# Kernel optimization log

Measured on AMD Instinct MI355X. Metric: run time of the kernel, lower is better.

## Reference

```python
import jax, jax.numpy as jnp
import numpy as np

MAJOR = 100          # major_resolution
SAMPLE = 11          # sample_resolution (11x11 = 121 blur taps)
SCALE = 1.0          # sample_scale
N_SIGMA = 4.0
B, C, H, W = 16, 3, 256, 256


def _gaussian_blur_grid(n):
    # torch.linspace(-1,1,n+2)[1:-1], meshgrid indexing 'ij'
    lin = jnp.linspace(-1.0, 1.0, n + 2)[1:-1]
    xx, yy = jnp.meshgrid(lin, lin, indexing='ij')
    ww = jnp.exp(-0.5 * (xx * xx + yy * yy) * N_SIGMA ** 2)
    ww = ww / jnp.sum(ww)
    return xx.ravel(), yy.ravel(), ww.ravel()


def _grid_sample_bilinear_zeros(x, grid):
    """torch.nn.functional.grid_sample, mode='bilinear', padding_mode='zeros',
    align_corners=False. x: [B,C,H,W], grid: [B,Ho,Wo,2] (last dim = (x,y))."""
    _, _, h, w = x.shape
    # unnormalize (align_corners=False): pixel = ((g+1)*size - 1)/2
    ix = ((grid[..., 0] + 1.0) * w - 1.0) * 0.5
    iy = ((grid[..., 1] + 1.0) * h - 1.0) * 0.5
    ix0 = jnp.floor(ix)
    iy0 = jnp.floor(iy)
    ix1 = ix0 + 1.0
    iy1 = iy0 + 1.0
    wx1 = ix - ix0
    wx0 = 1.0 - wx1
    wy1 = iy - iy0
    wy0 = 1.0 - wy1

    def tap(iy_f, ix_f, wgt):
        valid = ((iy_f >= 0) & (iy_f <= h - 1) & (ix_f >= 0) & (ix_f <= w - 1)).astype(x.dtype)
        iyc = jnp.clip(iy_f.astype(jnp.int32), 0, h - 1)
        ixc = jnp.clip(ix_f.astype(jnp.int32), 0, w - 1)
        # gather per batch element: [C,H,W] indexed by [Ho,Wo] -> [C,Ho,Wo]
        g = jax.vmap(lambda img, a, b: img[:, a, b])(x, iyc, ixc)  # [B,C,Ho,Wo]
        return g * (wgt * valid)[:, None, :, :]

    return (tap(iy0, ix0, wy0 * wx0) + tap(iy0, ix1, wy0 * wx1)
            + tap(iy1, ix0, wy1 * wx0) + tap(iy1, ix1, wy1 * wx1))


def setup_inputs() -> dict:
    key = jax.random.key(0)
    k1, k2 = jax.random.split(key)
    x = jax.random.normal(k1, (B, C, H, W), dtype=jnp.float32)
    theta = jax.random.normal(k2, (B, 2, 3), dtype=jnp.float32)
    return {"x": x, "theta": theta}


def reference(x, theta):
    b, c, _, _ = x.shape
    m = MAJOR
    bx, by, bw = _gaussian_blur_grid(SAMPLE)
    scale = SCALE / (m - 1)
    # affine_grid base coords, align_corners=False pixel centers in [-1,1]
    lin = (jnp.arange(m, dtype=x.dtype) + 0.5) * (2.0 / m) - 1.0
    coords = jnp.stack([
        jnp.broadcast_to(lin[None, :], (m, m)),   # x varies along width
        jnp.broadcast_to(lin[:, None], (m, m)),   # y varies along height
        jnp.ones((m, m), x.dtype),
    ], axis=-1)  # [M,M,3]

    def step(acc, tap):
        dx, dy, wgt = tap
        # _shift_affine_grid: theta[:,:,2] += theta[:,:,0]*dx + theta[:,:,1]*dy
        th = theta.at[:, :, 2].add(theta[:, :, 0] * (dx * scale) + theta[:, :, 1] * (dy * scale))
        grid = jnp.einsum('bij,hwj->bhwi', th, coords)  # [B,M,M,2]
        acc = acc + wgt * _grid_sample_bilinear_zeros(x, grid)
        return acc, None

    out0 = jnp.zeros((b, c, m, m), x.dtype)
    out, _ = jax.lax.scan(step, out0, (bx, by, bw))
    return out
```

## Files before the change

kernel.cpp:

```cpp
#include <hip/hip_runtime.h>
#include <hip/hip_fp16.h>


#define BB 16
#define HWP 65536
#define SMEMN 3072

__device__ const unsigned char KEPT[112] = {
    2,   3,   4,   5,   6,   7,   8,
    12,  13,  14,  15,  16,  17,  18,  19,  20,
    22,  23,  24,  25,  26,  27,  28,  29,  30,  31,  32,
    33,  34,  35,  36,  37,  38,  39,  40,  41,  42,  43,
    44,  45,  46,  47,  48,  49,  50,  51,  52,  53,  54,
    55,  56,  57,  58,  59,  60,  61,  62,  63,  64,  65,
    66,  67,  68,  69,  70,  71,  72,  73,  74,  75,  76,
    77,  78,  79,  80,  81,  82,  83,  84,  85,  86,  87,
    88,  89,  90,  91,  92,  93,  94,  95,  96,  97,  98,
    100, 101, 102, 103, 104, 105, 106, 107, 108,
    112, 113, 114, 115, 116, 117, 118,
    255, 255, 255};

#define INV_SUMW 0.07076221f
#define PXSCALE 1.2929293f

__global__ __launch_bounds__(256) void stn_fused(const float* __restrict__ x,
                                                 const float* __restrict__ theta,
                                                 float* __restrict__ out) {
  __shared__ uint2 smem[SMEMN];

  int bid = blockIdx.x;
  int swz = (bid & 7) * 1250 + (bid >> 3);
  int tid = threadIdx.x;
  int sub = tid & 15;
  int grp = tid >> 4;

  int b = swz / 625;
  int tt = swz - b * 625;
  int ti = tt / 25, tj = tt - ti * 25;
  int i0 = ti * 4, j0 = tj * 4;
  int i = i0 + (grp >> 2), j = j0 + (grp & 3);

  const float* th = theta + b * 6;
  float th00 = th[0], th01 = th[1], th02 = th[2];
  float th10 = th[3], th11 = th[4], th12 = th[5];

  float linj = (j + 0.5f) * 0.02f - 1.0f;
  float lini = (i + 0.5f) * 0.02f - 1.0f;
  float bix = (th00 * linj + th01 * lini + th02) * 128.0f + 127.5f;
  float biy = (th10 * linj + th11 * lini + th12) * 128.0f + 127.5f;

  float lj0 = (j0 + 0.5f) * 0.02f - 1.0f, lj3 = (j0 + 3.5f) * 0.02f - 1.0f;
  float li0 = (i0 + 0.5f) * 0.02f - 1.0f, li3 = (i0 + 3.5f) * 0.02f - 1.0f;
  float cx00 = th00 * lj0 + th01 * li0, cx01 = th00 * lj3 + th01 * li0;
  float cx10 = th00 * lj0 + th01 * li3, cx11 = th00 * lj3 + th01 * li3;
  float cy00 = th10 * lj0 + th11 * li0, cy01 = th10 * lj3 + th11 * li0;
  float cy10 = th10 * lj0 + th11 * li3, cy11 = th10 * lj3 + th11 * li3;
  float bxm = (fminf(fminf(cx00, cx01), fminf(cx10, cx11)) + th02) * 128.0f + 127.5f;
  float bxM = (fmaxf(fmaxf(cx00, cx01), fmaxf(cx10, cx11)) + th02) * 128.0f + 127.5f;
  float bym = (fminf(fminf(cy00, cy01), fminf(cy10, cy11)) + th12) * 128.0f + 127.5f;
  float byM = (fmaxf(fmaxf(cy00, cy01), fmaxf(cy10, cy11)) + th12) * 128.0f + 127.5f;
  float rx = 1.0775f * (fabsf(th00) + fabsf(th01));
  float ry = 1.0775f * (fabsf(th10) + fabsf(th11));
  int X0 = (int)floorf(bxm - rx) - 1;
  int X1 = (int)floorf(bxM + rx) + 2;
  int Y0 = (int)floorf(bym - ry) - 1;
  int Y1 = (int)floorf(byM + ry) + 2;
  int wreg = X1 - X0 + 1, hreg = Y1 - Y0 + 1;
  bool fast = (wreg <= 64) && (hreg <= 96) && (wreg * hreg <= SMEMN);

  float a00 = th00 * PXSCALE, a01 = th01 * PXSCALE;
  float a10 = th10 * PXSCALE, a11 = th11 * PXSCALE;
  float offx[7], offy[7], wk[7];
#pragma unroll
  for (int k = 0; k < 7; ++k) {
    int t = KEPT[sub + 16 * k];
    float dxk = 0.f, dyk = 0.f, wkk = 0.f;
    if (t != 255) {
      int s = t / 11, u = t - s * 11;
      dxk = (float)(s + 1) * 0.16666667f - 1.0f;
      dyk = (float)(u + 1) * 0.16666667f - 1.0f;
      wkk = __expf(-8.0f * (dxk * dxk + dyk * dyk)) * INV_SUMW;
    }
    offx[k] = a00 * dxk + a01 * dyk;
    offy[k] = a10 * dxk + a11 * dyk;
    wk[k] = wkk;
  }

  float acc0 = 0.f, acc1 = 0.f, acc2 = 0.f;
  const float* xb = x + (size_t)b * 3 * HWP;

  if (fast) {
    int c = tid & 63;
    for (int r = tid >> 6; r < hreg; r += 4) {
      if (c < wreg) {
        int py = Y0 + r, px = X0 + c;
        float v0 = 0.f, v1 = 0.f, v2 = 0.f;
        if ((unsigned)py < 256u && (unsigned)px < 256u) {
          int o = py * 256 + px;
          v0 = xb[o];
          v1 = xb[o + HWP];
          v2 = xb[o + 2 * HWP];
        }
        uint2 pkd;
        pkd.x = __builtin_bit_cast(unsigned, __floats2half2_rn(v0, v1));
        pkd.y = __builtin_bit_cast(unsigned, __floats2half2_rn(v2, 0.f));
        smem[r * wreg + c] = pkd;
      }
    }
    __syncthreads();

#pragma unroll
    for (int k = 0; k < 7; ++k) {
      float ixf = bix + offx[k];
      float iyf = biy + offy[k];
      float xf0 = floorf(ixf), yf0 = floorf(iyf);
      float fx = ixf - xf0, fy = iyf - yf0;
      int idx = ((int)yf0 - Y0) * wreg + ((int)xf0 - X0);
      uint2 A0 = smem[idx];
      uint2 A1 = smem[idx + 1];
      uint2 B0 = smem[idx + wreg];
      uint2 B1 = smem[idx + wreg + 1];
      float vb = wk[k] * fx;
      float waf = wk[k] - vb;
      __half2 wa2 = __float2half2_rn(waf);
      __half2 wb2 = __float2half2_rn(vb);
      __half2 wy0 = __float2half2_rn(1.0f - fy);
      __half2 wy1 = __float2half2_rn(fy);
      __half2 a0 = __builtin_bit_cast(__half2, A0.x);
      __half2 a1 = __builtin_bit_cast(__half2, A0.y);
      __half2 a2 = __builtin_bit_cast(__half2, A1.x);
      __half2 a3 = __builtin_bit_cast(__half2, A1.y);
      __half2 b0 = __builtin_bit_cast(__half2, B0.x);
      __half2 b1 = __builtin_bit_cast(__half2, B0.y);
      __half2 b2 = __builtin_bit_cast(__half2, B1.x);
      __half2 b3 = __builtin_bit_cast(__half2, B1.y);
      __half2 r0c01 = __hfma2(a2, wb2, __hmul2(a0, wa2));
      __half2 r0c2  = __hfma2(a3, wb2, __hmul2(a1, wa2));
      __half2 r1c01 = __hfma2(b2, wb2, __hmul2(b0, wa2));
      __half2 r1c2  = __hfma2(b3, wb2, __hmul2(b1, wa2));
      __half2 o01 = __hfma2(r1c01, wy1, __hmul2(r0c01, wy0));
      __half2 o2  = __hfma2(r1c2,  wy1, __hmul2(r0c2,  wy0));
      acc0 += __low2float(o01);
      acc1 += __high2float(o01);
      acc2 += __low2float(o2);
    }
  } else {
#pragma unroll 1
    for (int k = 0; k < 7; ++k) {
      float ixf = bix + offx[k];
      float iyf = biy + offy[k];
      float xf0 = floorf(ixf), yf0 = floorf(iyf);
      float fx = ixf - xf0, fy = iyf - yf0;
      int ix0 = (int)xf0, iy0 = (int)yf0;
      int ix1 = ix0 + 1, iy1 = iy0 + 1;
      float wx0 = ((unsigned)ix0 < 256u) ? (1.0f - fx) : 0.0f;
      float wx1 = ((unsigned)ix1 < 256u) ? fx : 0.0f;
      float wy0 = ((unsigned)iy0 < 256u) ? (1.0f - fy) : 0.0f;
      float wy1 = ((unsigned)iy1 < 256u) ? fy : 0.0f;
      int x0c = min(max(ix0, 0), 255);
      int x1c = min(max(ix1, 0), 255);
      int y0c = min(max(iy0, 0), 255);
      int y1c = min(max(iy1, 0), 255);
      float w00 = wk[k] * wy0 * wx0;
      float w01 = wk[k] * wy0 * wx1;
      float w10 = wk[k] * wy1 * wx0;
      float w11 = wk[k] * wy1 * wx1;
      int a00i = y0c * 256 + x0c, a01i = y0c * 256 + x1c;
      int a10i = y1c * 256 + x0c, a11i = y1c * 256 + x1c;
      acc0 += w00 * xb[a00i] + w01 * xb[a01i] + w10 * xb[a10i] + w11 * xb[a11i];
      const float* xb1 = xb + HWP;
      acc1 += w00 * xb1[a00i] + w01 * xb1[a01i] + w10 * xb1[a10i] + w11 * xb1[a11i];
      const float* xb2 = xb + 2 * HWP;
      acc2 += w00 * xb2[a00i] + w01 * xb2[a01i] + w10 * xb2[a10i] + w11 * xb2[a11i];
    }
  }

#pragma unroll
  for (int m = 1; m < 16; m <<= 1) {
    acc0 += __shfl_xor(acc0, m, 64);
    acc1 += __shfl_xor(acc1, m, 64);
    acc2 += __shfl_xor(acc2, m, 64);
  }

  if (sub == 0) {
    float* ob = out + (size_t)b * 30000 + i * 100 + j;
    ob[0] = acc0;
    ob[10000] = acc1;
    ob[20000] = acc2;
  }
}

extern "C" void kernel_launch(void* const* d_in, const int* in_sizes, int n_in,
                              void* d_out, int out_size, void* d_ws, size_t ws_size,
                              hipStream_t stream) {
  const float* x = (const float*)d_in[0];
  const float* theta = (const float*)d_in[1];
  float* out = (float*)d_out;
  (void)d_ws; (void)ws_size;
  stn_fused<<<10000, 256, 0, stream>>>(x, theta, out);
}
```

Baseline: 97.67 us.

## Vectorize halo staging with float2 loads, padded stride, early-exit, shared tap table

Staging of the input halo into LDS now loads two adjacent pixels per thread with float2 reads, using an even-aligned region start and clamped addresses, and writes 16-byte packed entries with a padded row stride meant to reduce bank conflicts. Tiles whose footprint lies entirely outside the image now write zeros and exit early. Per-tap offsets and weights are computed once per block into a shared table rather than seven times per thread. The blur weight normalisation constant also changes. The shared table adds a barrier on the slow path and extra LDS reads per tap.

```diff
diff --git a/kernel.cpp b/kernel.cpp
--- a/kernel.cpp
+++ b/kernel.cpp
@@ -20,13 +20,14 @@
     112, 113, 114, 115, 116, 117, 118,
     255, 255, 255};
 
-#define INV_SUMW 0.07076221f
+#define INV_SUMW 0.0707666f
 #define PXSCALE 1.2929293f
 
 __global__ __launch_bounds__(256) void stn_fused(const float* __restrict__ x,
                                                  const float* __restrict__ theta,
                                                  float* __restrict__ out) {
   __shared__ uint2 smem[SMEMN];
+  __shared__ float4 stab[112];
 
   int bid = blockIdx.x;
   int swz = (bid & 7) * 1250 + (bid >> 3);
@@ -61,19 +62,28 @@
   float byM = (fmaxf(fmaxf(cy00, cy01), fmaxf(cy10, cy11)) + th12) * 128.0f + 127.5f;
   float rx = 1.0775f * (fabsf(th00) + fabsf(th01));
   float ry = 1.0775f * (fabsf(th10) + fabsf(th11));
-  int X0 = (int)floorf(bxm - rx) - 1;
+  int X0 = ((int)floorf(bxm - rx) - 1) & ~1;
   int X1 = (int)floorf(bxM + rx) + 2;
   int Y0 = (int)floorf(bym - ry) - 1;
   int Y1 = (int)floorf(byM + ry) + 2;
-  int wreg = X1 - X0 + 1, hreg = Y1 - Y0 + 1;
-  bool fast = (wreg <= 64) && (hreg <= 96) && (wreg * hreg <= SMEMN);
+  int wreg = (X1 - X0 + 2) & ~1;
+  int sreg = wreg + 1;
+  int hreg = Y1 - Y0 + 1;
+
+  if (X1 < 0 || X0 > 255 || Y1 < 0 || Y0 > 255) {
+    if (sub == 0) {
+      float* ob = out + (size_t)b * 30000 + i * 100 + j;
+      ob[0] = 0.f; ob[10000] = 0.f; ob[20000] = 0.f;
+    }
+    return;
+  }
+
+  bool fast = (wreg <= 64) && (hreg <= 96) && (hreg * sreg <= SMEMN);
 
   float a00 = th00 * PXSCALE, a01 = th01 * PXSCALE;
   float a10 = th10 * PXSCALE, a11 = th11 * PXSCALE;
-  float offx[7], offy[7], wk[7];
-#pragma unroll
-  for (int k = 0; k < 7; ++k) {
-    int t = KEPT[sub + 16 * k];
+  if (tid < 112) {
+    int t = KEPT[tid];
     float dxk = 0.f, dyk = 0.f, wkk = 0.f;
     if (t != 255) {
       int s = t / 11, u = t - s * 11;
@@ -81,47 +91,53 @@
       dyk = (float)(u + 1) * 0.16666667f - 1.0f;
       wkk = __expf(-8.0f * (dxk * dxk + dyk * dyk)) * INV_SUMW;
     }
-    offx[k] = a00 * dxk + a01 * dyk;
-    offy[k] = a10 * dxk + a11 * dyk;
-    wk[k] = wkk;
+    stab[tid] = make_float4(a00 * dxk + a01 * dyk, a10 * dxk + a11 * dyk, wkk, 0.f);
   }
 
-  float acc0 = 0.f, acc1 = 0.f, acc2 = 0.f;
   const float* xb = x + (size_t)b * 3 * HWP;
 
   if (fast) {
-    int c = tid & 63;
-    for (int r = tid >> 6; r < hreg; r += 4) {
+    int c = (tid & 31) << 1;
+    for (int r = tid >> 5; r < hreg; r += 8) {
       if (c < wreg) {
-        int py = Y0 + r, px = X0 + c;
-        float v0 = 0.f, v1 = 0.f, v2 = 0.f;
-        if ((unsigned)py < 256u && (unsigned)px < 256u) {
-          int o = py * 256 + px;
-          v0 = xb[o];
-          v1 = xb[o + HWP];
-          v2 = xb[o + 2 * HWP];
-        }
-        uint2 pkd;
-        pkd.x = __builtin_bit_cast(unsigned, __floats2half2_rn(v0, v1));
-        pkd.y = __builtin_bit_cast(unsigned, __floats2half2_rn(v2, 0.f));
-        smem[r * wreg + c] = pkd;
+        int py = Y0 + r;
+        int px = X0 + c;
+        int pyc = min(max(py, 0), 255);
+        int pxc = min(max(px, 0), 254);
+        const float* src = xb + pyc * 256 + pxc;
+        float2 c0 = *(const float2*)(src);
+        float2 c1 = *(const float2*)(src + HWP);
+        float2 c2 = *(const float2*)(src + 2 * HWP);
+        bool rok = (unsigned)py < 256u;
+        bool m0 = rok && ((unsigned)px < 256u);
+        bool m1 = rok && ((unsigned)(px + 1) < 256u);
+        float v00 = m0 ? c0.x : 0.f, v01 = m0 ? c1.x : 0.f, v02 = m0 ? c2.x : 0.f;
+        float v10 = m1 ? c0.y : 0.f, v11 = m1 ? c1.y : 0.f, v12 = m1 ? c2.y : 0.f;
+        uint4 pkd;
+        pkd.x = __builtin_bit_cast(unsigned, __floats2half2_rn(v00, v01));
+        pkd.y = __builtin_bit_cast(unsigned, __floats2half2_rn(v02, 0.f));
+        pkd.z = __builtin_bit_cast(unsigned, __floats2half2_rn(v10, v11));
+        pkd.w = __builtin_bit_cast(unsigned, __floats2half2_rn(v12, 0.f));
+        *(uint4*)(&smem[r * sreg + c]) = pkd;
       }
     }
     __syncthreads();
 
+    float acc0 = 0.f, acc1 = 0.f, acc2 = 0.f;
 #pragma unroll
     for (int k = 0; k < 7; ++k) {
-      float ixf = bix + offx[k];
-      float iyf = biy + offy[k];
+      float4 tv = stab[sub + 16 * k];
+      float ixf = bix + tv.x;
+      float iyf = biy + tv.y;
       float xf0 = floorf(ixf), yf0 = floorf(iyf);
       float fx = ixf - xf0, fy = iyf - yf0;
-      int idx = ((int)yf0 - Y0) * wreg + ((int)xf0 - X0);
+      int idx = ((int)yf0 - Y0) * sreg + ((int)xf0 - X0);
       uint2 A0 = smem[idx];
       uint2 A1 = smem[idx + 1];
-      uint2 B0 = smem[idx + wreg];
-      uint2 B1 = smem[idx + wreg + 1];
-      float vb = wk[k] * fx;
-      float waf = wk[k] - vb;
+      uint2 B0 = smem[idx + sreg];
+      uint2 B1 = smem[idx + sreg + 1];
+      float vb = tv.z * fx;
+      float waf = tv.z - vb;
       __half2 wa2 = __float2half2_rn(waf);
       __half2 wb2 = __float2half2_rn(vb);
       __half2 wy0 = __float2half2_rn(1.0f - fy);
@@ -144,11 +160,25 @@
       acc1 += __high2float(o01);
       acc2 += __low2float(o2);
     }
+
+#pragma unroll
+    for (int m = 1; m < 16; m <<= 1) {
+      acc0 += __shfl_xor(acc0, m, 64);
+      acc1 += __shfl_xor(acc1, m, 64);
+      acc2 += __shfl_xor(acc2, m, 64);
+    }
+    if (sub == 0) {
+      float* ob = out + (size_t)b * 30000 + i * 100 + j;
+      ob[0] = acc0; ob[10000] = acc1; ob[20000] = acc2;
+    }
   } else {
+    __syncthreads();
+    float acc0 = 0.f, acc1 = 0.f, acc2 = 0.f;
 #pragma unroll 1
     for (int k = 0; k < 7; ++k) {
-      float ixf = bix + offx[k];
-      float iyf = biy + offy[k];
+      float4 tv = stab[sub + 16 * k];
+      float ixf = bix + tv.x;
+      float iyf = biy + tv.y;
       float xf0 = floorf(ixf), yf0 = floorf(iyf);
       float fx = ixf - xf0, fy = iyf - yf0;
       int ix0 = (int)xf0, iy0 = (int)yf0;
@@ -161,10 +191,10 @@
       int x1c = min(max(ix1, 0), 255);
       int y0c = min(max(iy0, 0), 255);
       int y1c = min(max(iy1, 0), 255);
-      float w00 = wk[k] * wy0 * wx0;
-      float w01 = wk[k] * wy0 * wx1;
-      float w10 = wk[k] * wy1 * wx0;
-      float w11 = wk[k] * wy1 * wx1;
+      float w00 = tv.z * wy0 * wx0;
+      float w01 = tv.z * wy0 * wx1;
+      float w10 = tv.z * wy1 * wx0;
+      float w11 = tv.z * wy1 * wx1;
       int a00i = y0c * 256 + x0c, a01i = y0c * 256 + x1c;
       int a10i = y1c * 256 + x0c, a11i = y1c * 256 + x1c;
       acc0 += w00 * xb[a00i] + w01 * xb[a01i] + w10 * xb[a10i] + w11 * xb[a11i];
@@ -173,20 +203,16 @@
       const float* xb2 = xb + 2 * HWP;
       acc2 += w00 * xb2[a00i] + w01 * xb2[a01i] + w10 * xb2[a10i] + w11 * xb2[a11i];
     }
-  }
-
 #pragma unroll
-  for (int m = 1; m < 16; m <<= 1) {
-    acc0 += __shfl_xor(acc0, m, 64);
-    acc1 += __shfl_xor(acc1, m, 64);
-    acc2 += __shfl_xor(acc2, m, 64);
-  }
-
-  if (sub == 0) {
-    float* ob = out + (size_t)b * 30000 + i * 100 + j;
-    ob[0] = acc0;
-    ob[10000] = acc1;
-    ob[20000] = acc2;
+    for (int m = 1; m < 16; m <<= 1) {
+      acc0 += __shfl_xor(acc0, m, 64);
+      acc1 += __shfl_xor(acc1, m, 64);
+      acc2 += __shfl_xor(acc2, m, 64);
+    }
+    if (sub == 0) {
+      float* ob = out + (size_t)b * 30000 + i * 100 + j;
+      ob[0] = acc0; ob[10000] = acc1; ob[20000] = acc2;
+    }
   }
 }
 
```

New measurement: 79.19 us. 18.9% less time.
